# Kernel optimization log

Measured on AMD Instinct MI355X. Metric: run time of the kernel, lower is better.

## Reference

```python
import jax, jax.numpy as jnp
import numpy as np

B, S, D, H = 4, 2048, 1024, 16
DK = D // H


def _rope(x):
    # x: [B, H, S, DK]; lucidrains rotary_embedding_torch default:
    # theta=10000, interleaved (rotate_half on (d/2, 2) pairs), freqs repeated pairwise.
    s, d = x.shape[-2], x.shape[-1]
    inv_freq = 1.0 / (10000.0 ** (jnp.arange(0, d, 2, dtype=jnp.float32) / d))  # [d/2]
    angles = jnp.arange(s, dtype=jnp.float32)[:, None] * inv_freq[None, :]      # [S, d/2]
    ang = jnp.repeat(angles, 2, axis=-1)                                        # [S, d] interleaved
    cos, sin = jnp.cos(ang), jnp.sin(ang)
    xp = x.reshape(*x.shape[:-1], d // 2, 2)
    rot = jnp.stack((-xp[..., 1], xp[..., 0]), axis=-1).reshape(x.shape)        # rotate_half
    return x * cos + rot * sin


def setup_inputs() -> dict:
    key = jax.random.key(0)
    ks = jax.random.split(key, 8)
    scale = 1.0 / np.sqrt(D)
    return {
        "q": jax.random.normal(ks[0], (B, S, D), dtype=jnp.float32),
        "k": jax.random.normal(ks[1], (B, S, D), dtype=jnp.float32),
        "v": jax.random.normal(ks[2], (B, S, D), dtype=jnp.float32),
        "mask": jax.random.randint(ks[3], (B, S), 0, 2, dtype=jnp.int32),
        "w_q": jax.random.normal(ks[4], (D, D), dtype=jnp.float32) * scale,
        "w_k": jax.random.normal(ks[5], (D, D), dtype=jnp.float32) * scale,
        "w_v": jax.random.normal(ks[6], (D, D), dtype=jnp.float32) * scale,
        "w_o": jax.random.normal(ks[7], (D, D), dtype=jnp.float32) * scale,
    }


def reference(q, k, v, mask, w_q, w_k, w_v, w_o):
    # Linear weights stored [out, in] as in torch; y = x @ W^T (bias=False).
    def split_heads(x):
        b, s, _ = x.shape
        return x.reshape(b, s, H, DK).transpose(0, 2, 1, 3)  # [B,H,S,DK]

    query = split_heads(q @ w_q.T)
    key_ = split_heads(k @ w_k.T)
    value = split_heads(v @ w_v.T)

    query = _rope(query)
    key_ = _rope(key_)

    scores = jnp.einsum("bhqd,bhkd->bhqk", query, key_) / np.sqrt(DK)
    scores = jnp.where(mask[:, None, None, :] == 0, -10000.0, scores)
    attn = jax.nn.softmax(scores, axis=-1)  # dropout is identity at eval
    x = jnp.einsum("bhqk,bhkd->bhqd", attn, value)
    x = x.transpose(0, 2, 1, 3).reshape(q.shape[0], -1, H * DK)
    return x @ w_o.T
```

## Files before the change

### kernel.cpp

```cpp
#include <hip/hip_runtime.h>
#include <hip/hip_bf16.h>
#include <math.h>


namespace {

constexpr int Bb = 4, Ss = 2048, Dd = 1024, Hh = 16, DKk = 64;
constexpr size_t NElem = (size_t)Bb * Hh * Ss * DKk;
constexpr size_t WElem = (size_t)Dd * Dd;

typedef __bf16 bf16;
typedef __attribute__((ext_vector_type(8))) __bf16 bf16x8;
typedef __attribute__((ext_vector_type(4))) float f32x4;

__device__ __forceinline__ bf16x8 pack8(float4 a, float4 b) {
  bf16x8 r;
  r[0] = (__bf16)a.x; r[1] = (__bf16)a.y; r[2] = (__bf16)a.z; r[3] = (__bf16)a.w;
  r[4] = (__bf16)b.x; r[5] = (__bf16)b.y; r[6] = (__bf16)b.z; r[7] = (__bf16)b.w;
  return r;
}

__device__ __forceinline__ void gl_lds16(const bf16* g, bf16* l) {
  __builtin_amdgcn_global_load_lds((const __attribute__((address_space(1))) void*)g,
                                   (__attribute__((address_space(3))) void*)l, 16, 0, 0);
}

__global__ __launch_bounds__(256) void cvt6(const float* __restrict__ q,
                                            const float* __restrict__ k,
                                            const float* __restrict__ v,
                                            const float* __restrict__ wq,
                                            const float* __restrict__ wk,
                                            const float* __restrict__ wv,
                                            bf16* __restrict__ xd, bf16* __restrict__ wd) {
  const int bid = blockIdx.x;
  const float* s; bf16* d; size_t idx;
  if (bid < 12288) {
    const int t = bid >> 12;
    s = (t == 0) ? q : (t == 1) ? k : v;
    d = xd + (size_t)t * NElem;
    idx = ((size_t)(bid & 4095) * 256 + threadIdx.x) * 8;
  } else {
    const int t = (bid - 12288) >> 9;
    s = (t == 0) ? wq : (t == 1) ? wk : wv;
    d = wd + (size_t)t * WElem;
    idx = ((size_t)((bid - 12288) & 511) * 256 + threadIdx.x) * 8;
  }
  float4 f0 = *(const float4*)(s + idx), f1 = *(const float4*)(s + idx + 4);
  *(bf16x8*)(d + idx) = pack8(f0, f1);
}

__global__ __launch_bounds__(256) void cvt_pair(const float* __restrict__ x, bf16* __restrict__ xd,
                                                const float* __restrict__ ws, bf16* __restrict__ wd) {
  const int bid = blockIdx.x;
  const float* s; bf16* d; size_t idx;
  if (bid < 4096) { s = x; d = xd; idx = (size_t)bid * 256 + threadIdx.x; }
  else { s = ws; d = wd; idx = (size_t)(bid - 4096) * 256 + threadIdx.x; }
  idx *= 8;
  float4 f0 = *(const float4*)(s + idx), f1 = *(const float4*)(s + idx + 4);
  *(bf16x8*)(d + idx) = pack8(f0, f1);
}

__global__ __launch_bounds__(256) void cvt_w(const float* __restrict__ ws, bf16* __restrict__ wd) {
  size_t idx = ((size_t)blockIdx.x * 256 + threadIdx.x) * 8;
  float4 f0 = *(const float4*)(ws + idx), f1 = *(const float4*)(ws + idx + 4);
  *(bf16x8*)(wd + idx) = pack8(f0, f1);
}

template <int MODE>
__global__ __launch_bounds__(256, 4) void mha_gemm(const bf16* __restrict__ A,
                                                   const bf16* __restrict__ W,
                                                   void* __restrict__ dstv) {
  __shared__ __align__(16) bf16 As[2][128][32];
  __shared__ __align__(16) bf16 Bs[2][128][32];
  const int tid = threadIdx.x;
  const int z = (MODE == 3) ? blockIdx.z : 0;
  const int bm0 = blockIdx.x * 128, bn0 = blockIdx.y * 128;
  const int w = tid >> 6, lane = tid & 63, l16 = lane & 15, quad = lane >> 4;
  const int wm = (w >> 1) * 64, wn = (w & 1) * 64;
  const int lr = lane >> 2, lc = (lane & 3) * 8;

  const bf16* Ag = A + (size_t)z * NElem + (size_t)(bm0 + w * 32 + lr) * Dd + lc;
  const bf16* Wg = W + (size_t)z * WElem + (size_t)(bn0 + w * 32 + lr) * Dd + lc;

  f32x4 acc[4][4] = {};

  gl_lds16(Ag, &As[0][w * 32][0]);
  gl_lds16(Ag + 16 * Dd, &As[0][w * 32 + 16][0]);
  gl_lds16(Wg, &Bs[0][w * 32][0]);
  gl_lds16(Wg + 16 * Dd, &Bs[0][w * 32 + 16][0]);
  __syncthreads();

  for (int kt = 0; kt < 32; ++kt) {
    const int cur = kt & 1, nxt = cur ^ 1;
    if (kt < 31) {
      const int ko = (kt + 1) * 32;
      gl_lds16(Ag + ko, &As[nxt][w * 32][0]);
      gl_lds16(Ag + ko + 16 * Dd, &As[nxt][w * 32 + 16][0]);
      gl_lds16(Wg + ko, &Bs[nxt][w * 32][0]);
      gl_lds16(Wg + ko + 16 * Dd, &Bs[nxt][w * 32 + 16][0]);
    }
    bf16x8 af[4], bw[4];
#pragma unroll
    for (int i = 0; i < 4; ++i) af[i] = *(bf16x8*)&As[cur][wm + i * 16 + l16][quad * 8];
#pragma unroll
    for (int i = 0; i < 4; ++i) bw[i] = *(bf16x8*)&Bs[cur][wn + i * 16 + l16][quad * 8];
#pragma unroll
    for (int mt = 0; mt < 4; ++mt)
#pragma unroll
      for (int nt = 0; nt < 4; ++nt)
        acc[mt][nt] =
            __builtin_amdgcn_mfma_f32_16x16x32_bf16(af[mt], bw[nt], acc[mt][nt], 0, 0, 0);
    __syncthreads();
  }

  const bool do_rope = (MODE == 0) || (MODE == 3 && z < 2);
  const bool do_vt = (MODE == 1) || (MODE == 3 && z == 2);

  if constexpr (MODE == 2) {
    float* out = (float*)dstv;
#pragma unroll
    for (int mt = 0; mt < 4; ++mt)
#pragma unroll
      for (int nt = 0; nt < 4; ++nt) {
        const int gcol = bn0 + wn + nt * 16 + l16;
        const int grow0 = bm0 + wm + mt * 16 + quad * 4;
#pragma unroll
        for (int r = 0; r < 4; ++r) out[(size_t)(grow0 + r) * Dd + gcol] = acc[mt][nt][r];
      }
  } else {
    if (do_vt) {
      bf16* vt = (bf16*)dstv + (MODE == 3 ? 2 * NElem : 0);
#pragma unroll
      for (int mt = 0; mt < 4; ++mt)
#pragma unroll
        for (int nt = 0; nt < 4; ++nt) {
          const int gcol = bn0 + wn + nt * 16 + l16;
          const int h = gcol >> 6, dk = gcol & 63;
#pragma unroll
          for (int r = 0; r < 4; ++r) {
            const int grow = bm0 + wm + mt * 16 + quad * 4 + r;
            const int b = grow >> 11, s = grow & (Ss - 1);
            vt[((size_t)(b * Hh + h) * DKk + dk) * Ss + s] = (bf16)acc[mt][nt][r];
          }
        }
    } else if (do_rope) {
      bf16* qp = (bf16*)dstv + (MODE == 3 ? (size_t)z * NElem : 0);
#pragma unroll
      for (int mt = 0; mt < 4; ++mt)
#pragma unroll
        for (int nt = 0; nt < 4; ++nt) {
          const int gcol = bn0 + wn + nt * 16 + l16;
          const int h = gcol >> 6, dk = gcol & 63;
          const float invf = exp2f((float)(dk >> 1) * -0.4152410118609203f);
          const float sgn = (dk & 1) ? 1.0f : -1.0f;
#pragma unroll
          for (int r = 0; r < 4; ++r) {
            const int grow = bm0 + wm + mt * 16 + quad * 4 + r;
            const int b = grow >> 11, s = grow & (Ss - 1);
            const float v = acc[mt][nt][r];
            const float ov = __shfl_xor(v, 1);
            float sn, cs;
            __sincosf((float)s * invf, &sn, &cs);
            const float rot = v * cs + sgn * ov * sn;
            qp[((size_t)(b * Hh + h) * Ss + s) * DKk + dk] = (bf16)rot;
          }
        }
    }
  }
}

__global__ __launch_bounds__(256, 4) void mha_attn(const bf16* __restrict__ Qp,
                                                   const bf16* __restrict__ Kp,
                                                   const bf16* __restrict__ Vt,
                                                   const int* __restrict__ maskG,
                                                   bf16* __restrict__ Xo) {
  __shared__ __align__(16) bf16 Ks[2][64][64];
  __shared__ __align__(16) bf16 Vs[2][64][64];
  __shared__ __align__(16) bf16 Pbuf[4][1024];

  constexpr float c1 = 0.18033688011112042f;
  constexpr float c2 = -17.312340490667562f;

  const int tid = threadIdx.x;
  const int bh = blockIdx.y, b = bh >> 4, h = bh & 15;
  const int q0 = blockIdx.x * 128;
  const int w = tid >> 6, lane = tid & 63, l16 = lane & 15, quad = lane >> 4;
  const int swz = l16 & 7;
  const size_t hbase = (size_t)bh * Ss * DKk;

  {
    bf16* Qst = &Ks[0][0][0];
    const int row = tid >> 1, hf = tid & 1;
    const bf16* src = Qp + hbase + (size_t)(q0 + row) * DKk + hf * 32;
#pragma unroll
    for (int cc = 0; cc < 4; ++cc)
      *(int4*)&Qst[(((hf * 4 + cc) * 128) + row) * 8] = *(const int4*)(src + cc * 8);
  }
  __syncthreads();
  bf16x8 qf[2][2];
  {
    const bf16* Qst = &Ks[0][0][0];
#pragma unroll
    for (int mt = 0; mt < 2; ++mt)
#pragma unroll
      for (int kk = 0; kk < 2; ++kk)
        qf[mt][kk] = *(bf16x8*)&Qst[(((kk * 4 + quad) * 128) + w * 32 + mt * 16 + l16) * 8];
  }
  __syncthreads();

  const int srow = lane >> 3, schunk = (lane & 7) ^ (srow & 7);
  const bf16* Kg = Kp + hbase + (size_t)(w * 16 + srow) * DKk + schunk * 8;
  const bf16* Vg = Vt + ((size_t)bh * DKk + w * 16 + srow) * Ss + schunk * 8;
  const int* Mg = maskG + b * Ss + l16;

  int mcur[4], mnext[4];
#pragma unroll
  for (int i = 0; i < 2; ++i) {
    gl_lds16(Kg + (size_t)i * 8 * DKk, &Ks[0][w * 16 + i * 8][0]);
    gl_lds16(Vg + i * 8 * Ss, &Vs[0][w * 16 + i * 8][0]);
  }
#pragma unroll
  for (int nt = 0; nt < 4; ++nt) mcur[nt] = Mg[nt * 16];
  __syncthreads();

  f32x4 o[2][4] = {};
  f32x4 lo[2] = {};
  bf16* Pb = &Pbuf[w][0];

  bf16x8 vones;
#pragma unroll
  for (int i = 0; i < 8; ++i) vones[i] = (__bf16)1.0f;

  for (int kt = 0; kt < 32; ++kt) {
    const int cur = kt & 1, nxt = cur ^ 1;
    if (kt < 31) {
      const size_t k0n = (size_t)(kt + 1) * 64;
#pragma unroll
      for (int i = 0; i < 2; ++i) {
        gl_lds16(Kg + k0n * DKk + (size_t)i * 8 * DKk, &Ks[nxt][w * 16 + i * 8][0]);
        gl_lds16(Vg + k0n + i * 8 * Ss, &Vs[nxt][w * 16 + i * 8][0]);
      }
#pragma unroll
      for (int nt = 0; nt < 4; ++nt) mnext[nt] = Mg[k0n + nt * 16];
    }

    f32x4 sc[2][4];
#pragma unroll
    for (int nt = 0; nt < 4; ++nt) {
      const float bv = (mcur[nt] != 0) ? 0.0f : -1e9f;
#pragma unroll
      for (int r = 0; r < 4; ++r) { sc[0][nt][r] = bv; sc[1][nt][r] = bv; }
    }
#pragma unroll
    for (int kk = 0; kk < 2; ++kk)
#pragma unroll
      for (int nt = 0; nt < 4; ++nt) {
        bf16x8 kf = *(bf16x8*)&Ks[cur][nt * 16 + l16][((kk * 4 + quad) ^ swz) * 8];
        sc[0][nt] = __builtin_amdgcn_mfma_f32_16x16x32_bf16(qf[0][kk], kf, sc[0][nt], 0, 0, 0);
        sc[1][nt] = __builtin_amdgcn_mfma_f32_16x16x32_bf16(qf[1][kk], kf, sc[1][nt], 0, 0, 0);
      }

    bf16x8 pf0[2], pf1[2];
#pragma unroll
    for (int nt = 0; nt < 4; ++nt) {
      const int c = nt * 2 + (l16 >> 3);
      const int jj = l16 & 7;
#pragma unroll
      for (int r = 0; r < 4; ++r)
        Pb[(c * 16 + quad * 4 + r) * 8 + jj] = (bf16)exp2f(fmaf(sc[0][nt][r], c1, c2));
    }
#pragma unroll
    for (int kk = 0; kk < 2; ++kk)
      pf0[kk] = *(bf16x8*)(Pb + ((kk * 4 + quad) * 16 + l16) * 8);
#pragma unroll
    for (int nt = 0; nt < 4; ++nt) {
      const int c = nt * 2 + (l16 >> 3);
      const int jj = l16 & 7;
#pragma unroll
      for (int r = 0; r < 4; ++r)
        Pb[(c * 16 + quad * 4 + r) * 8 + jj] = (bf16)exp2f(fmaf(sc[1][nt][r], c1, c2));
    }
#pragma unroll
    for (int kk = 0; kk < 2; ++kk)
      pf1[kk] = *(bf16x8*)(Pb + ((kk * 4 + quad) * 16 + l16) * 8);

#pragma unroll
    for (int kk = 0; kk < 2; ++kk) {
      lo[0] = __builtin_amdgcn_mfma_f32_16x16x32_bf16(pf0[kk], vones, lo[0], 0, 0, 0);
      lo[1] = __builtin_amdgcn_mfma_f32_16x16x32_bf16(pf1[kk], vones, lo[1], 0, 0, 0);
#pragma unroll
      for (int nt = 0; nt < 4; ++nt) {
        bf16x8 vf = *(bf16x8*)&Vs[cur][nt * 16 + l16][((kk * 4 + quad) ^ swz) * 8];
        o[0][nt] = __builtin_amdgcn_mfma_f32_16x16x32_bf16(pf0[kk], vf, o[0][nt], 0, 0, 0);
        o[1][nt] = __builtin_amdgcn_mfma_f32_16x16x32_bf16(pf1[kk], vf, o[1][nt], 0, 0, 0);
      }
    }
    __syncthreads();
#pragma unroll
    for (int nt = 0; nt < 4; ++nt) mcur[nt] = mnext[nt];
  }

#pragma unroll
  for (int mt = 0; mt < 2; ++mt)
#pragma unroll
    for (int nt = 0; nt < 4; ++nt)
#pragma unroll
      for (int r = 0; r < 4; ++r) {
        const int srw = q0 + w * 32 + mt * 16 + quad * 4 + r;
        const int dk = nt * 16 + l16;
        Xo[(size_t)(b * Ss + srw) * Dd + h * DKk + dk] = (bf16)(o[mt][nt][r] / lo[mt][r]);
      }
}

}

extern "C" void kernel_launch(void* const* d_in, const int* in_sizes, int n_in,
                              void* d_out, int out_size, void* d_ws, size_t ws_size,
                              hipStream_t stream) {
  (void)in_sizes; (void)n_in; (void)out_size;
  const float* q = (const float*)d_in[0];
  const float* k = (const float*)d_in[1];
  const float* v = (const float*)d_in[2];
  const int* mask = (const int*)d_in[3];
  const float* w_q = (const float*)d_in[4];
  const float* w_k = (const float*)d_in[5];
  const float* w_v = (const float*)d_in[6];
  const float* w_o = (const float*)d_in[7];
  float* out = (float*)d_out;

  dim3 blk(256);
  const size_t fused_bytes = (6 * NElem + 3 * WElem) * sizeof(bf16);

  if (ws_size >= fused_bytes) {
    bf16* Ab = (bf16*)d_ws;
    bf16* Wb = Ab + 3 * NElem;
    bf16* Db = Wb + 3 * WElem;
    bf16* Qp = Db;
    bf16* Kp = Db + NElem;
    bf16* Vt = Db + 2 * NElem;
    bf16* Xo = Ab;

    cvt6<<<13824, blk, 0, stream>>>(q, k, v, w_q, w_k, w_v, Ab, Wb);
    mha_gemm<3><<<dim3(64, 8, 3), blk, 0, stream>>>(Ab, Wb, (void*)Db);
    mha_attn<<<dim3(16, 64), blk, 0, stream>>>(Qp, Kp, Vt, mask, Xo);
    cvt_w<<<512, blk, 0, stream>>>(w_o, Wb);
    mha_gemm<2><<<dim3(64, 8), blk, 0, stream>>>(Xo, Wb, (void*)out);
  } else {
    bf16* buf0 = (bf16*)d_ws;
    bf16* wbuf = buf0 + NElem;
    bf16* Qp = wbuf + WElem;
    bf16* Kp = Qp + NElem;
    bf16* Vt = Kp + NElem;

    dim3 g(64, 8);
    cvt_pair<<<4608, blk, 0, stream>>>(q, buf0, w_q, wbuf);
    mha_gemm<0><<<g, blk, 0, stream>>>(buf0, wbuf, (void*)Qp);
    cvt_pair<<<4608, blk, 0, stream>>>(k, buf0, w_k, wbuf);
    mha_gemm<0><<<g, blk, 0, stream>>>(buf0, wbuf, (void*)Kp);
    cvt_pair<<<4608, blk, 0, stream>>>(v, buf0, w_v, wbuf);
    mha_gemm<1><<<g, blk, 0, stream>>>(buf0, wbuf, (void*)Vt);
    mha_attn<<<dim3(16, 64), blk, 0, stream>>>(Qp, Kp, Vt, mask, buf0);
    cvt_w<<<512, blk, 0, stream>>>(w_o, wbuf);
    mha_gemm<2><<<g, blk, 0, stream>>>(buf0, wbuf, (void*)out);
  }
}
```

Before: 376.6 us.

## Keep softmax probabilities in registers by computing transposed scores for PV MFMA

Swaps the operands of the QK^T MFMA so each lane holds score values in the layout needed as the A operand of a 16x16x16 bf16 MFMA for P·V. This removes the per-wave LDS round trip (Pbuf stores and reloads) used to reshape P, and the mask is now loaded as int4 per lane to match the transposed layout. In exchange the PV and row-sum MFMAs become twice as many, half-size 16x16x16 instructions with narrower V fragment reads, and launch bounds drop from 4 to 3 waves per SIMD, which may raise register headroom but lower occupancy.

New measurement: 394.6 us. +4.8%, slower.

```diff
diff --git a/kernel.cpp b/kernel.cpp
--- a/kernel.cpp
+++ b/kernel.cpp
@@ -12,6 +12,7 @@
 typedef __bf16 bf16;
 typedef __attribute__((ext_vector_type(8))) __bf16 bf16x8;
 typedef __attribute__((ext_vector_type(4))) float f32x4;
+typedef __attribute__((ext_vector_type(4))) short short4v;
 
 __device__ __forceinline__ bf16x8 pack8(float4 a, float4 b) {
   bf16x8 r;
@@ -169,14 +170,13 @@
   }
 }
 
-__global__ __launch_bounds__(256, 4) void mha_attn(const bf16* __restrict__ Qp,
+__global__ __launch_bounds__(256, 3) void mha_attn(const bf16* __restrict__ Qp,
                                                    const bf16* __restrict__ Kp,
                                                    const bf16* __restrict__ Vt,
                                                    const int* __restrict__ maskG,
                                                    bf16* __restrict__ Xo) {
   __shared__ __align__(16) bf16 Ks[2][64][64];
   __shared__ __align__(16) bf16 Vs[2][64][64];
-  __shared__ __align__(16) bf16 Pbuf[4][1024];
 
   constexpr float c1 = 0.18033688011112042f;
   constexpr float c2 = -17.312340490667562f;
@@ -211,25 +211,24 @@
   const int srow = lane >> 3, schunk = (lane & 7) ^ (srow & 7);
   const bf16* Kg = Kp + hbase + (size_t)(w * 16 + srow) * DKk + schunk * 8;
   const bf16* Vg = Vt + ((size_t)bh * DKk + w * 16 + srow) * Ss + schunk * 8;
-  const int* Mg = maskG + b * Ss + l16;
-
-  int mcur[4], mnext[4];
+  const int* Mg = maskG + b * Ss + quad * 4;
+
+  int4 mcur[4], mnext[4];
 #pragma unroll
   for (int i = 0; i < 2; ++i) {
     gl_lds16(Kg + (size_t)i * 8 * DKk, &Ks[0][w * 16 + i * 8][0]);
     gl_lds16(Vg + i * 8 * Ss, &Vs[0][w * 16 + i * 8][0]);
   }
 #pragma unroll
-  for (int nt = 0; nt < 4; ++nt) mcur[nt] = Mg[nt * 16];
+  for (int nt = 0; nt < 4; ++nt) mcur[nt] = *(const int4*)(Mg + nt * 16);
   __syncthreads();
 
   f32x4 o[2][4] = {};
   f32x4 lo[2] = {};
-  bf16* Pb = &Pbuf[w][0];
-
-  bf16x8 vones;
-#pragma unroll
-  for (int i = 0; i < 8; ++i) vones[i] = (__bf16)1.0f;
+
+  short4v ones4;
+#pragma unroll
+  for (int i = 0; i < 4; ++i) ones4[i] = (short)0x3F80;
 
   for (int kt = 0; kt < 32; ++kt) {
     const int cur = kt & 1, nxt = cur ^ 1;
@@ -241,58 +240,51 @@
         gl_lds16(Vg + k0n + i * 8 * Ss, &Vs[nxt][w * 16 + i * 8][0]);
       }
 #pragma unroll
-      for (int nt = 0; nt < 4; ++nt) mnext[nt] = Mg[k0n + nt * 16];
+      for (int nt = 0; nt < 4; ++nt) mnext[nt] = *(const int4*)(Mg + k0n + nt * 16);
     }
 
     f32x4 sc[2][4];
 #pragma unroll
     for (int nt = 0; nt < 4; ++nt) {
-      const float bv = (mcur[nt] != 0) ? 0.0f : -1e9f;
-#pragma unroll
-      for (int r = 0; r < 4; ++r) { sc[0][nt][r] = bv; sc[1][nt][r] = bv; }
+      const int4 m4 = mcur[nt];
+      const float bv0 = (m4.x != 0) ? 0.0f : -1e9f;
+      const float bv1 = (m4.y != 0) ? 0.0f : -1e9f;
+      const float bv2 = (m4.z != 0) ? 0.0f : -1e9f;
+      const float bv3 = (m4.w != 0) ? 0.0f : -1e9f;
+      sc[0][nt][0] = bv0; sc[0][nt][1] = bv1; sc[0][nt][2] = bv2; sc[0][nt][3] = bv3;
+      sc[1][nt][0] = bv0; sc[1][nt][1] = bv1; sc[1][nt][2] = bv2; sc[1][nt][3] = bv3;
     }
 #pragma unroll
     for (int kk = 0; kk < 2; ++kk)
 #pragma unroll
       for (int nt = 0; nt < 4; ++nt) {
         bf16x8 kf = *(bf16x8*)&Ks[cur][nt * 16 + l16][((kk * 4 + quad) ^ swz) * 8];
-        sc[0][nt] = __builtin_amdgcn_mfma_f32_16x16x32_bf16(qf[0][kk], kf, sc[0][nt], 0, 0, 0);
-        sc[1][nt] = __builtin_amdgcn_mfma_f32_16x16x32_bf16(qf[1][kk], kf, sc[1][nt], 0, 0, 0);
-      }
-
-    bf16x8 pf0[2], pf1[2];
-#pragma unroll
-    for (int nt = 0; nt < 4; ++nt) {
-      const int c = nt * 2 + (l16 >> 3);
-      const int jj = l16 & 7;
-#pragma unroll
-      for (int r = 0; r < 4; ++r)
-        Pb[(c * 16 + quad * 4 + r) * 8 + jj] = (bf16)exp2f(fmaf(sc[0][nt][r], c1, c2));
-    }
-#pragma unroll
-    for (int kk = 0; kk < 2; ++kk)
-      pf0[kk] = *(bf16x8*)(Pb + ((kk * 4 + quad) * 16 + l16) * 8);
-#pragma unroll
-    for (int nt = 0; nt < 4; ++nt) {
-      const int c = nt * 2 + (l16 >> 3);
-      const int jj = l16 & 7;
-#pragma unroll
-      for (int r = 0; r < 4; ++r)
-        Pb[(c * 16 + quad * 4 + r) * 8 + jj] = (bf16)exp2f(fmaf(sc[1][nt][r], c1, c2));
-    }
-#pragma unroll
-    for (int kk = 0; kk < 2; ++kk)
-      pf1[kk] = *(bf16x8*)(Pb + ((kk * 4 + quad) * 16 + l16) * 8);
-
-#pragma unroll
-    for (int kk = 0; kk < 2; ++kk) {
-      lo[0] = __builtin_amdgcn_mfma_f32_16x16x32_bf16(pf0[kk], vones, lo[0], 0, 0, 0);
-      lo[1] = __builtin_amdgcn_mfma_f32_16x16x32_bf16(pf1[kk], vones, lo[1], 0, 0, 0);
-#pragma unroll
-      for (int nt = 0; nt < 4; ++nt) {
-        bf16x8 vf = *(bf16x8*)&Vs[cur][nt * 16 + l16][((kk * 4 + quad) ^ swz) * 8];
-        o[0][nt] = __builtin_amdgcn_mfma_f32_16x16x32_bf16(pf0[kk], vf, o[0][nt], 0, 0, 0);
-        o[1][nt] = __builtin_amdgcn_mfma_f32_16x16x32_bf16(pf1[kk], vf, o[1][nt], 0, 0, 0);
+        sc[0][nt] = __builtin_amdgcn_mfma_f32_16x16x32_bf16(kf, qf[0][kk], sc[0][nt], 0, 0, 0);
+        sc[1][nt] = __builtin_amdgcn_mfma_f32_16x16x32_bf16(kf, qf[1][kk], sc[1][nt], 0, 0, 0);
+      }
+
+    short4v pa[2][4];
+#pragma unroll
+    for (int mt = 0; mt < 2; ++mt)
+#pragma unroll
+      for (int nt = 0; nt < 4; ++nt)
+#pragma unroll
+        for (int r = 0; r < 4; ++r) {
+          const float pv = exp2f(fmaf(sc[mt][nt][r], c1, c2));
+          const __bf16 tb = (__bf16)pv;
+          pa[mt][nt][r] = __builtin_bit_cast(short, tb);
+        }
+
+#pragma unroll
+    for (int ks = 0; ks < 4; ++ks) {
+      lo[0] = __builtin_amdgcn_mfma_f32_16x16x16bf16_1k(pa[0][ks], ones4, lo[0], 0, 0, 0);
+      lo[1] = __builtin_amdgcn_mfma_f32_16x16x16bf16_1k(pa[1][ks], ones4, lo[1], 0, 0, 0);
+#pragma unroll
+      for (int dt = 0; dt < 4; ++dt) {
+        const short4v vb = *(const short4v*)&Vs[cur][dt * 16 + l16]
+                                               [(((ks * 2 + (quad >> 1)) ^ swz) * 8 + (quad & 1) * 4)];
+        o[0][dt] = __builtin_amdgcn_mfma_f32_16x16x16bf16_1k(pa[0][ks], vb, o[0][dt], 0, 0, 0);
+        o[1][dt] = __builtin_amdgcn_mfma_f32_16x16x16bf16_1k(pa[1][ks], vb, o[1][dt], 0, 0, 0);
       }
     }
     __syncthreads();
@@ -303,12 +295,12 @@
 #pragma unroll
   for (int mt = 0; mt < 2; ++mt)
 #pragma unroll
-    for (int nt = 0; nt < 4; ++nt)
+    for (int dt = 0; dt < 4; ++dt)
 #pragma unroll
       for (int r = 0; r < 4; ++r) {
         const int srw = q0 + w * 32 + mt * 16 + quad * 4 + r;
-        const int dk = nt * 16 + l16;
-        Xo[(size_t)(b * Ss + srw) * Dd + h * DKk + dk] = (bf16)(o[mt][nt][r] / lo[mt][r]);
+        const int dk = dt * 16 + l16;
+        Xo[(size_t)(b * Ss + srw) * Dd + h * DKk + dk] = (bf16)(o[mt][dt][r] / lo[mt][r]);
       }
 }
 
```
